# Optimization experiments

Measured on AMD Instinct MI355X. Metric: run time of the kernel, lower is better.

Reference implementation:

```python
import jax, jax.numpy as jnp
import numpy as np

N_NODES = 50000
N_EDGES = 1600000
F_NODE = 8
F_EDGE = 4
HIDDEN = 16
OUT = 8
MLP_HID = 25


def _nnconv(x, src, dst, edge_attr, wa, ba, wb, bb, root, bias, out_ch):
    # edge MLP -> per-edge weight matrix [E, in_ch, out_ch]
    h = jax.nn.relu(edge_attr @ wa + ba) @ wb + bb
    w = h.reshape(-1, x.shape[1], out_ch)
    # gather source node feats, per-edge small matmul
    msg = jnp.einsum('ei,eio->eo', x[src], w)  # [E, out_ch]
    n = x.shape[0]
    agg = jax.ops.segment_sum(msg, dst, num_segments=n)
    cnt = jax.ops.segment_sum(jnp.ones((msg.shape[0],), msg.dtype), dst, num_segments=n)
    agg = agg / jnp.maximum(cnt, 1.0)[:, None]  # mean aggregation
    return agg + x @ root + bias  # root weight + bias (PyG NNConv defaults)


def setup_inputs() -> dict:
    key = jax.random.key(0)
    ks = jax.random.split(key, 16)
    s = lambda k, shape, fan: jax.random.normal(k, shape, jnp.float32) * (1.0 / np.sqrt(fan))
    return {
        'x': jax.random.normal(ks[0], (N_NODES, F_NODE), jnp.float32),
        'edge_index': jax.random.randint(ks[1], (2, N_EDGES), 0, N_NODES),
        'edge_attr': jax.random.normal(ks[2], (N_EDGES, F_EDGE), jnp.float32),
        # conv1 edge-MLP: F_EDGE -> 25 -> F_NODE*HIDDEN
        'w1a': s(ks[3], (F_EDGE, MLP_HID), F_EDGE), 'b1a': jnp.zeros((MLP_HID,), jnp.float32),
        'w1b': s(ks[4], (MLP_HID, F_NODE * HIDDEN), MLP_HID), 'b1b': jnp.zeros((F_NODE * HIDDEN,), jnp.float32),
        'root1': s(ks[5], (F_NODE, HIDDEN), F_NODE), 'bias1': jnp.zeros((HIDDEN,), jnp.float32),
        # conv2 edge-MLP: F_EDGE -> 25 -> HIDDEN*OUT
        'w2a': s(ks[6], (F_EDGE, MLP_HID), F_EDGE), 'b2a': jnp.zeros((MLP_HID,), jnp.float32),
        'w2b': s(ks[7], (MLP_HID, HIDDEN * OUT), MLP_HID), 'b2b': jnp.zeros((HIDDEN * OUT,), jnp.float32),
        'root2': s(ks[8], (HIDDEN, OUT), HIDDEN), 'bias2': jnp.zeros((OUT,), jnp.float32),
    }


def reference(x, edge_index, edge_attr, w1a, b1a, w1b, b1b, root1, bias1,
              w2a, b2a, w2b, b2b, root2, bias2):
    src, dst = edge_index[0], edge_index[1]
    h = _nnconv(x, src, dst, edge_attr, w1a, b1a, w1b, b1b, root1, bias1, HIDDEN)
    h = jax.nn.relu(h)
    # dropout p=0.5 is identity in eval mode
    out = _nnconv(h, src, dst, edge_attr, w2a, b2a, w2b, b2b, root2, bias2, OUT)
    return out
```

## Files before the change

### kernel.cpp

```cpp
#include <hip/hip_runtime.h>
#include <hip/hip_fp16.h>

#define NN 50000
#define NE 1600000
#define FN 8
#define FE 4
#define HID 16
#define OC 8
#define MH 25
#define CAP 80
#define BINS 196
#define BCAP 8960
#define TILE 4096


typedef int iv4 __attribute__((ext_vector_type(4)));
static __device__ __forceinline__ int4 ntload4(const int4* p) {
    iv4 v = __builtin_nontemporal_load(reinterpret_cast<const iv4*>(p));
    return make_int4(v.x, v.y, v.z, v.w);
}
static __device__ __forceinline__ unsigned pack2h(float lo, float hi) {
    return ((unsigned)__half_as_ushort(__float2half_rn(hi)) << 16)
         |  (unsigned)__half_as_ushort(__float2half_rn(lo));
}

#define PKFMA_LO(acc, a, b) \
    asm("v_pk_fma_f16 %0, %1, %2, %0 op_sel:[0,0,0] op_sel_hi:[0,1,1]" \
        : "+v"(acc) : "v"(a), "v"(b))
#define PKFMA_HI(acc, a, b) \
    asm("v_pk_fma_f16 %0, %1, %2, %0 op_sel:[1,0,0] op_sel_hi:[1,1,1]" \
        : "+v"(acc) : "v"(a), "v"(b))
#define PKMAX0(dst, a) \
    asm("v_pk_max_f16 %0, %1, 0" : "=v"(dst) : "v"(a))

static __device__ __forceinline__ void unpack2(unsigned u, float& lo, float& hi) {
    __half2 h; *reinterpret_cast<unsigned*>(&h) = u;
    float2 f = __half22float2(h);
    lo = f.x; hi = f.y;
}

__global__ void __launch_bounds__(256) xhalf_kernel(const float4* __restrict__ x4,
                                                    uint4* __restrict__ xh4) {
    int n = blockIdx.x * 256 + threadIdx.x;
    if (n < NN) {
        float4 a = x4[2 * n], b = x4[2 * n + 1];
        xh4[n] = make_uint4(pack2h(a.x, a.y), pack2h(a.z, a.w),
                            pack2h(b.x, b.y), pack2h(b.z, b.w));
    }
}

__global__ void __launch_bounds__(256) binA_kernel(
    const int* __restrict__ ei, const float* __restrict__ ea,
    unsigned* __restrict__ gcursor, int4* __restrict__ binbuf) {
    __shared__ unsigned hist[BINS], basei[BINS], run[BINS];
    for (int t = threadIdx.x; t < BINS; t += 256) { hist[t] = 0u; run[t] = 0u; }
    __syncthreads();
    const int bb = blockIdx.x * TILE;
    int dsts[16], srcs[16];
    bool actk[4];
#pragma unroll
    for (int k = 0; k < 4; ++k) {
        int e = bb + k * 1024 + threadIdx.x * 4;
        actk[k] = e < NE;
        int4 d = make_int4(0, 0, 0, 0), s = make_int4(0, 0, 0, 0);
        if (actk[k]) {
            d = *reinterpret_cast<const int4*>(ei + NE + e);
            s = *reinterpret_cast<const int4*>(ei + e);
        }
        dsts[4 * k]     = d.x; dsts[4 * k + 1] = d.y;
        dsts[4 * k + 2] = d.z; dsts[4 * k + 3] = d.w;
        srcs[4 * k]     = s.x; srcs[4 * k + 1] = s.y;
        srcs[4 * k + 2] = s.z; srcs[4 * k + 3] = s.w;
        if (actk[k]) {
            atomicAdd(&hist[d.x >> 8], 1u);
            atomicAdd(&hist[d.y >> 8], 1u);
            atomicAdd(&hist[d.z >> 8], 1u);
            atomicAdd(&hist[d.w >> 8], 1u);
        }
    }
    __syncthreads();
    for (int t = threadIdx.x; t < BINS; t += 256)
        basei[t] = hist[t] ? atomicAdd(&gcursor[t], hist[t]) : 0u;
    __syncthreads();
#pragma unroll
    for (int k = 0; k < 4; ++k) {
        if (!actk[k]) continue;
        int e = bb + k * 1024 + threadIdx.x * 4;
#pragma unroll
        for (int j = 0; j < 4; ++j) {
            float4 a = *reinterpret_cast<const float4*>(ea + 4ull * (e + j));
            unsigned u01 = pack2h(a.x, a.y);
            unsigned u23 = pack2h(a.z, a.w);
            int d = dsts[4 * k + j];
            int b = d >> 8;
            unsigned off = atomicAdd(&run[b], 1u);
            unsigned slot = basei[b] + off;
            if (slot < BCAP)
                binbuf[(size_t)b * BCAP + slot] =
                    make_int4(srcs[4 * k + j], d, (int)u01, (int)u23);
        }
    }
}

__global__ void __launch_bounds__(512) binB_kernel(
    const int4* __restrict__ binbuf, const unsigned* __restrict__ gcursor,
    unsigned* __restrict__ cursorF, int4* __restrict__ recs) {
    int b   = blockIdx.x >> 2;
    int sub = blockIdx.x & 3;
    unsigned cnt = gcursor[b];
    if (cnt > BCAP) cnt = BCAP;
    const int4* srcp = binbuf + (size_t)b * BCAP;
    for (unsigned i = threadIdx.x + sub * 512u; i < cnt; i += 2048u) {
        int4 r = ntload4(srcp + i);
        int dst = r.y;
        unsigned pos = atomicAdd(&cursorF[dst], 1u);
        if (pos < CAP)
            recs[(size_t)dst * CAP + pos] = make_int4(r.x, r.z, r.w, 0);
    }
}

__global__ void __launch_bounds__(512, 8) conv1_kernel(
    const float* __restrict__ x, const __half* __restrict__ xh,
    const int4* __restrict__ recs, const unsigned* __restrict__ cnts,
    const float* __restrict__ wa, const float* __restrict__ ba,
    const float* __restrict__ wb, const float* __restrict__ bb,
    const float* __restrict__ root, const float* __restrict__ bias,
    float* __restrict__ hn)
{
    __shared__ float s_wa[FE * MH];
    __shared__ float s_ba[MH];
    __shared__ float s_wb[26 * 129];
    __shared__ float s_root[FN * HID];
    __shared__ float s_bias[HID];
    __shared__ uint2 s_ea[8][4][17];
    __shared__ uint4 s_g[8][4][17];
    for (int t = threadIdx.x; t < FE * MH; t += 512) s_wa[t] = wa[t];
    for (int t = threadIdx.x; t < MH; t += 512) s_ba[t] = ba[t];
    for (int t = threadIdx.x; t < 26 * 128; t += 512) {
        int r = t >> 7, c = t & 127;
        s_wb[r * 129 + c] = (r < MH) ? wb[t] : bb[c];
    }
    for (int t = threadIdx.x; t < FN * HID; t += 512) s_root[t] = root[t];
    for (int t = threadIdx.x; t < HID; t += 512) s_bias[t] = bias[t];
    {
        float* pg = reinterpret_cast<float*>(&s_g[0][0][0]);
        for (int t = threadIdx.x; t < 8 * 4 * 17 * 4; t += 512) pg[t] = 0.f;
    }
    __syncthreads();

    const float4* x4 = reinterpret_cast<const float4*>(x);
    const int w = threadIdx.x >> 6;
    const int l = threadIdx.x & 63;
    const int q = l >> 4;
    const int m = l & 15;
    const int n = blockIdx.x * 32 + w * 4 + q;
    const unsigned cnt = (n < NN) ? cnts[n] : 0u;
    const unsigned lim = cnt < CAP ? cnt : (unsigned)CAP;
    const size_t base = (size_t)n * CAP;
    unsigned cm = lim;
    cm = max(cm, (unsigned)__shfl_xor((int)cm, 16));
    cm = max(cm, (unsigned)__shfl_xor((int)cm, 32));

    const int m2 = m + 16;
    float wB0 = 0.f, wB1 = 0.f, wB2 = 0.f, wB3 = 0.f, bB = 0.f;
    if (m2 < MH) { wB0 = s_wa[m2]; wB1 = s_wa[MH + m2]; wB2 = s_wa[2 * MH + m2];
                   wB3 = s_wa[3 * MH + m2]; bB = s_ba[m2]; }
    else if (m2 == MH) bB = 1.f;
    const unsigned wAB0 = pack2h(s_wa[m], wB0);
    const unsigned wAB1 = pack2h(s_wa[MH + m], wB1);
    const unsigned wAB2 = pack2h(s_wa[2 * MH + m], wB2);
    const unsigned wAB3 = pack2h(s_wa[3 * MH + m], wB3);
    const unsigned bAB  = pack2h(s_ba[m], bB);

    unsigned TA[4] = {0u,0u,0u,0u}, TB[4] = {0u,0u,0u,0u};
    for (unsigned c = 0; c < cm; c += 16) {
        if (c + (unsigned)m < lim) {
            int4 r = ntload4(&recs[base + c + m]);
            s_ea[w][q][m] = make_uint2((unsigned)r.y, (unsigned)r.z);
            s_g[w][q][m] = *reinterpret_cast<const uint4*>(xh + 8ull * r.x);
        }
        asm volatile("s_waitcnt lgkmcnt(0)" ::: "memory");
#pragma unroll 4
        for (int j = 0; j < 16; ++j) {
            uint2 eu = s_ea[w][q][j];
            uint4 gu = s_g[w][q][j];
            unsigned hm2 = bAB;
            PKFMA_LO(hm2, eu.x, wAB0);
            PKFMA_HI(hm2, eu.x, wAB1);
            PKFMA_LO(hm2, eu.y, wAB2);
            PKFMA_HI(hm2, eu.y, wAB3);
            PKMAX0(hm2, hm2);
            bool act = (c + (unsigned)j) < lim;
            hm2 = act ? hm2 : 0u;
            PKFMA_LO(TA[0], hm2, gu.x); PKFMA_LO(TA[1], hm2, gu.y);
            PKFMA_LO(TA[2], hm2, gu.z); PKFMA_LO(TA[3], hm2, gu.w);
            PKFMA_HI(TB[0], hm2, gu.x); PKFMA_HI(TB[1], hm2, gu.y);
            PKFMA_HI(TB[2], hm2, gu.z); PKFMA_HI(TB[3], hm2, gu.w);
        }
        asm volatile("" ::: "memory");
    }

    float T[8], U[8];
    unpack2(TA[0], T[0], T[1]); unpack2(TA[1], T[2], T[3]);
    unpack2(TA[2], T[4], T[5]); unpack2(TA[3], T[6], T[7]);
    unpack2(TB[0], U[0], U[1]); unpack2(TB[1], U[2], U[3]);
    unpack2(TB[2], U[4], U[5]); unpack2(TB[3], U[6], U[7]);

    const int rb = (m2 <= MH) ? m2 : MH;
    float s[16];
#pragma unroll
    for (int o = 0; o < 16; ++o) {
        const float* wv = s_wb + m * 129 + o;
        const float* wu = s_wb + rb * 129 + o;
        float pm = T[0]*wv[0]  + T[1]*wv[16] + T[2]*wv[32] + T[3]*wv[48]
                 + T[4]*wv[64] + T[5]*wv[80] + T[6]*wv[96] + T[7]*wv[112]
                 + U[0]*wu[0]  + U[1]*wu[16] + U[2]*wu[32] + U[3]*wu[48]
                 + U[4]*wu[64] + U[5]*wu[80] + U[6]*wu[96] + U[7]*wu[112];
        pm += __shfl_xor(pm, 8, 16);
        pm += __shfl_xor(pm, 4, 16);
        pm += __shfl_xor(pm, 2, 16);
        pm += __shfl_xor(pm, 1, 16);
        s[o] = pm;
    }

    if (m == 0 && n < NN) {
        float inv = 1.f / fmaxf((float)cnt, 1.f);
        float4 xa = x4[2 * n], xb = x4[2 * n + 1];
        float xn[8] = {xa.x, xa.y, xa.z, xa.w, xb.x, xb.y, xb.z, xb.w};
        float v[16];
#pragma unroll
        for (int o = 0; o < 16; ++o) {
            float r = s[o] * inv + s_bias[o];
#pragma unroll
            for (int i = 0; i < 8; ++i) r += xn[i] * s_root[i * HID + o];
            v[o] = fmaxf(r, 0.f);
        }
        float4* hp = reinterpret_cast<float4*>(hn + 16ull * n);
        hp[0] = make_float4(v[0], v[1], v[2], v[3]);
        hp[1] = make_float4(v[4], v[5], v[6], v[7]);
        hp[2] = make_float4(v[8], v[9], v[10], v[11]);
        hp[3] = make_float4(v[12], v[13], v[14], v[15]);
    }
}

__global__ void __launch_bounds__(256) hn2h_kernel(const float4* __restrict__ hn4,
                                                   uint4* __restrict__ hh4) {
    int n = blockIdx.x * 256 + threadIdx.x;
    if (n < NN) {
        float4 a = hn4[4 * n],     b = hn4[4 * n + 1];
        float4 c = hn4[4 * n + 2], d = hn4[4 * n + 3];
        hh4[2 * n]     = make_uint4(pack2h(a.x, a.y), pack2h(a.z, a.w),
                                    pack2h(b.x, b.y), pack2h(b.z, b.w));
        hh4[2 * n + 1] = make_uint4(pack2h(c.x, c.y), pack2h(c.z, c.w),
                                    pack2h(d.x, d.y), pack2h(d.z, d.w));
    }
}

__global__ void __launch_bounds__(512, 8) conv2_kernel(
    const __half* __restrict__ hh, const int4* __restrict__ recs,
    const unsigned* __restrict__ cnts,
    const float* __restrict__ wa, const float* __restrict__ ba,
    const float* __restrict__ wb, const float* __restrict__ bb,
    const float* __restrict__ root, const float* __restrict__ bias,
    float* __restrict__ out)
{
    __shared__ float s_wa[FE * MH];
    __shared__ float s_ba[MH];
    __shared__ float s_wb[26 * 129];
    __shared__ float s_root[HID * OC];
    __shared__ float s_bias[OC];
    __shared__ uint2 s_ea[8][4][17];
    __shared__ uint4 s_gA[8][4][17];
    __shared__ uint4 s_gB[8][4][17];
    for (int t = threadIdx.x; t < FE * MH; t += 512) s_wa[t] = wa[t];
    for (int t = threadIdx.x; t < MH; t += 512) s_ba[t] = ba[t];
    for (int t = threadIdx.x; t < 26 * 128; t += 512) {
        int r = t >> 7, c = t & 127;
        s_wb[r * 129 + c] = (r < MH) ? wb[t] : bb[c];
    }
    for (int t = threadIdx.x; t < HID * OC; t += 512) s_root[t] = root[t];
    for (int t = threadIdx.x; t < OC; t += 512) s_bias[t] = bias[t];
    {
        float* pg = reinterpret_cast<float*>(&s_gA[0][0][0]);
        for (int t = threadIdx.x; t < 8 * 4 * 17 * 4; t += 512) pg[t] = 0.f;
        float* ph = reinterpret_cast<float*>(&s_gB[0][0][0]);
        for (int t = threadIdx.x; t < 8 * 4 * 17 * 4; t += 512) ph[t] = 0.f;
    }
    __syncthreads();

    const int w = threadIdx.x >> 6;
    const int l = threadIdx.x & 63;
    const int q = l >> 4;
    const int m = l & 15;
    const int n = blockIdx.x * 32 + w * 4 + q;
    const unsigned cnt = (n < NN) ? cnts[n] : 0u;
    const unsigned lim = cnt < CAP ? cnt : (unsigned)CAP;
    const size_t base = (size_t)n * CAP;
    unsigned cm = lim;
    cm = max(cm, (unsigned)__shfl_xor((int)cm, 16));
    cm = max(cm, (unsigned)__shfl_xor((int)cm, 32));

    const int m2 = m + 16;
    float wB0 = 0.f, wB1 = 0.f, wB2 = 0.f, wB3 = 0.f, bB = 0.f;
    if (m2 < MH) { wB0 = s_wa[m2]; wB1 = s_wa[MH + m2]; wB2 = s_wa[2 * MH + m2];
                   wB3 = s_wa[3 * MH + m2]; bB = s_ba[m2]; }
    else if (m2 == MH) bB = 1.f;
    const unsigned wAB0 = pack2h(s_wa[m], wB0);
    const unsigned wAB1 = pack2h(s_wa[MH + m], wB1);
    const unsigned wAB2 = pack2h(s_wa[2 * MH + m], wB2);
    const unsigned wAB3 = pack2h(s_wa[3 * MH + m], wB3);
    const unsigned bAB  = pack2h(s_ba[m], bB);

    unsigned TA[8] = {0u,0u,0u,0u,0u,0u,0u,0u};
    unsigned TB[8] = {0u,0u,0u,0u,0u,0u,0u,0u};
    for (unsigned c = 0; c < cm; c += 16) {
        if (c + (unsigned)m < lim) {
            int4 r = ntload4(&recs[base + c + m]);
            s_ea[w][q][m] = make_uint2((unsigned)r.y, (unsigned)r.z);
            const uint4* gp = reinterpret_cast<const uint4*>(hh + 16ull * r.x);
            s_gA[w][q][m] = gp[0];
            s_gB[w][q][m] = gp[1];
        }
        asm volatile("s_waitcnt lgkmcnt(0)" ::: "memory");
#pragma unroll 4
        for (int j = 0; j < 16; ++j) {
            uint2 eu = s_ea[w][q][j];
            uint4 ga = s_gA[w][q][j];
            uint4 gb = s_gB[w][q][j];
            unsigned hm2 = bAB;
            PKFMA_LO(hm2, eu.x, wAB0);
            PKFMA_HI(hm2, eu.x, wAB1);
            PKFMA_LO(hm2, eu.y, wAB2);
            PKFMA_HI(hm2, eu.y, wAB3);
            PKMAX0(hm2, hm2);
            bool act = (c + (unsigned)j) < lim;
            hm2 = act ? hm2 : 0u;
            PKFMA_LO(TA[0], hm2, ga.x); PKFMA_LO(TA[1], hm2, ga.y);
            PKFMA_LO(TA[2], hm2, ga.z); PKFMA_LO(TA[3], hm2, ga.w);
            PKFMA_LO(TA[4], hm2, gb.x); PKFMA_LO(TA[5], hm2, gb.y);
            PKFMA_LO(TA[6], hm2, gb.z); PKFMA_LO(TA[7], hm2, gb.w);
            PKFMA_HI(TB[0], hm2, ga.x); PKFMA_HI(TB[1], hm2, ga.y);
            PKFMA_HI(TB[2], hm2, ga.z); PKFMA_HI(TB[3], hm2, ga.w);
            PKFMA_HI(TB[4], hm2, gb.x); PKFMA_HI(TB[5], hm2, gb.y);
            PKFMA_HI(TB[6], hm2, gb.z); PKFMA_HI(TB[7], hm2, gb.w);
        }
        asm volatile("" ::: "memory");
    }

    float T[16], U[16];
#pragma unroll
    for (int i = 0; i < 8; ++i) {
        unpack2(TA[i], T[2 * i], T[2 * i + 1]);
        unpack2(TB[i], U[2 * i], U[2 * i + 1]);
    }

    const int rb = (m2 <= MH) ? m2 : MH;
    float s[8];
#pragma unroll
    for (int o = 0; o < 8; ++o) {
        const float* wv = s_wb + m * 129 + o;
        const float* wu = s_wb + rb * 129 + o;
        float pm = 0.f;
#pragma unroll
        for (int i = 0; i < 16; ++i) pm += T[i] * wv[i * 8];
#pragma unroll
        for (int i = 0; i < 16; ++i) pm += U[i] * wu[i * 8];
        pm += __shfl_xor(pm, 8, 16);
        pm += __shfl_xor(pm, 4, 16);
        pm += __shfl_xor(pm, 2, 16);
        pm += __shfl_xor(pm, 1, 16);
        s[o] = pm;
    }

    if (m == 0 && n < NN) {
        float inv = 1.f / fmaxf((float)cnt, 1.f);
        uint4 ha4 = *reinterpret_cast<const uint4*>(hh + 16ull * n);
        uint4 hb4 = *reinterpret_cast<const uint4*>(hh + 16ull * n + 8);
        const __half2* ap = reinterpret_cast<const __half2*>(&ha4);
        const __half2* bp = reinterpret_cast<const __half2*>(&hb4);
        float hnn[16];
#pragma unroll
        for (int i = 0; i < 4; ++i) {
            float2 fa = __half22float2(ap[i]);
            float2 fb = __half22float2(bp[i]);
            hnn[2 * i] = fa.x; hnn[2 * i + 1] = fa.y;
            hnn[8 + 2 * i] = fb.x; hnn[8 + 2 * i + 1] = fb.y;
        }
        float v[8];
#pragma unroll
        for (int o = 0; o < 8; ++o) {
            float r = s[o] * inv + s_bias[o];
#pragma unroll
            for (int i = 0; i < 16; ++i) r += hnn[i] * s_root[i * OC + o];
            v[o] = r;
        }
        float4* op = reinterpret_cast<float4*>(out + 8ull * n);
        op[0] = make_float4(v[0], v[1], v[2], v[3]);
        op[1] = make_float4(v[4], v[5], v[6], v[7]);
    }
}

extern "C" void kernel_launch(void* const* d_in, const int* in_sizes, int n_in,
                              void* d_out, int out_size, void* d_ws, size_t ws_size,
                              hipStream_t stream) {
    const float* x     = (const float*)d_in[0];
    const int*   ei    = (const int*)d_in[1];
    const float* ea    = (const float*)d_in[2];
    const float* w1a   = (const float*)d_in[3];
    const float* b1a   = (const float*)d_in[4];
    const float* w1b   = (const float*)d_in[5];
    const float* b1b   = (const float*)d_in[6];
    const float* root1 = (const float*)d_in[7];
    const float* bias1 = (const float*)d_in[8];
    const float* w2a   = (const float*)d_in[9];
    const float* b2a   = (const float*)d_in[10];
    const float* w2b   = (const float*)d_in[11];
    const float* b2b   = (const float*)d_in[12];
    const float* root2 = (const float*)d_in[13];
    const float* bias2 = (const float*)d_in[14];
    float* out = (float*)d_out;

    char* ws = (char*)d_ws;
    int4*     recs    = (int4*)(ws);
    unsigned* cursorF = (unsigned*)(ws + 64000000);
    unsigned* gcursor = (unsigned*)(ws + 64200000);
    float*    hn      = (float*)(ws + 64200800);
    __half*   hnh     = (__half*)(ws + 67400800);
    __half*   xh      = (__half*)(ws + 69000800);
    int4*     binbuf  = (int4*)(ws + 69800800);

    hipMemsetAsync(ws + 64000000, 0, 200784, stream);
    xhalf_kernel<<<(NN + 255) / 256, 256, 0, stream>>>((const float4*)x, (uint4*)xh);
    binA_kernel<<<(NE + TILE - 1) / TILE, 256, 0, stream>>>(ei, ea, gcursor, binbuf);
    binB_kernel<<<BINS * 4, 512, 0, stream>>>(binbuf, gcursor, cursorF, recs);
    conv1_kernel<<<(NN + 31) / 32, 512, 0, stream>>>(x, xh, recs, cursorF,
                                                     w1a, b1a, w1b, b1b, root1, bias1, hn);
    hn2h_kernel<<<(NN + 255) / 256, 256, 0, stream>>>((const float4*)hn, (uint4*)hnh);
    conv2_kernel<<<(NN + 31) / 32, 512, 0, stream>>>(hnh, recs, cursorF,
                                                     w2a, b2a, w2b, b2b, root2, bias2, out);
}
```

Before: 183.1 us.

## Stage binned edge records in LDS to coalesce binA scatter writes

binA now does a local prefix scan over the per-bin histogram and first scatters each tile's records into a shared-memory staging buffer grouped by bin. It then writes them out in bin order, so consecutive threads store to contiguous slots of each bin's global region instead of scattered addresses. Block size doubles to 512 threads with fewer edges per thread. The 64KB LDS stage and the extra barriers can lower occupancy.

Measured after the change: 177.7 us, median of 2. 1.03x faster.

```diff
diff --git a/kernel.cpp b/kernel.cpp
--- a/kernel.cpp
+++ b/kernel.cpp
@@ -49,18 +49,22 @@
     }
 }
 
-__global__ void __launch_bounds__(256) binA_kernel(
+__global__ void __launch_bounds__(512) binA_kernel(
     const int* __restrict__ ei, const float* __restrict__ ea,
     unsigned* __restrict__ gcursor, int4* __restrict__ binbuf) {
-    __shared__ unsigned hist[BINS], basei[BINS], run[BINS];
-    for (int t = threadIdx.x; t < BINS; t += 256) { hist[t] = 0u; run[t] = 0u; }
-    __syncthreads();
+    __shared__ unsigned hist[256], lstart[256], run[256], basei[256];
+    __shared__ unsigned scanbuf[256];
+    __shared__ int4 stage[TILE];
+    for (int t = threadIdx.x; t < 256; t += 512) { hist[t] = 0u; run[t] = 0u; }
+    __syncthreads();
+
     const int bb = blockIdx.x * TILE;
-    int dsts[16], srcs[16];
-    bool actk[4];
-#pragma unroll
-    for (int k = 0; k < 4; ++k) {
-        int e = bb + k * 1024 + threadIdx.x * 4;
+    const int tid = threadIdx.x;
+    int dsts[8], srcs[8];
+    bool actk[2];
+#pragma unroll
+    for (int k = 0; k < 2; ++k) {
+        int e = bb + k * 2048 + tid * 4;
         actk[k] = e < NE;
         int4 d = make_int4(0, 0, 0, 0), s = make_int4(0, 0, 0, 0);
         if (actk[k]) {
@@ -79,13 +83,23 @@
         }
     }
     __syncthreads();
-    for (int t = threadIdx.x; t < BINS; t += 256)
-        basei[t] = hist[t] ? atomicAdd(&gcursor[t], hist[t]) : 0u;
-    __syncthreads();
-#pragma unroll
-    for (int k = 0; k < 4; ++k) {
+    if (tid < 256) scanbuf[tid] = hist[tid];
+    __syncthreads();
+    for (int off = 1; off < 256; off <<= 1) {
+        unsigned v = 0u;
+        if (tid < 256 && tid >= off) v = scanbuf[tid - off];
+        __syncthreads();
+        if (tid < 256) scanbuf[tid] += v;
+        __syncthreads();
+    }
+    if (tid < 256) lstart[tid] = scanbuf[tid] - hist[tid];
+    if (tid < BINS) basei[tid] = hist[tid] ? atomicAdd(&gcursor[tid], hist[tid]) : 0u;
+    __syncthreads();
+
+#pragma unroll
+    for (int k = 0; k < 2; ++k) {
         if (!actk[k]) continue;
-        int e = bb + k * 1024 + threadIdx.x * 4;
+        int e = bb + k * 2048 + tid * 4;
 #pragma unroll
         for (int j = 0; j < 4; ++j) {
             float4 a = *reinterpret_cast<const float4*>(ea + 4ull * (e + j));
@@ -94,11 +108,17 @@
             int d = dsts[4 * k + j];
             int b = d >> 8;
             unsigned off = atomicAdd(&run[b], 1u);
-            unsigned slot = basei[b] + off;
-            if (slot < BCAP)
-                binbuf[(size_t)b * BCAP + slot] =
-                    make_int4(srcs[4 * k + j], d, (int)u01, (int)u23);
-        }
+            stage[lstart[b] + off] = make_int4(srcs[4 * k + j], d, (int)u01, (int)u23);
+        }
+    }
+    __syncthreads();
+
+    const int tot = (bb + TILE <= NE) ? TILE : (NE - bb);
+    for (int i = tid; i < tot; i += 512) {
+        int4 r = stage[i];
+        int b = r.y >> 8;
+        unsigned slot = basei[b] + ((unsigned)i - lstart[b]);
+        if (slot < BCAP) binbuf[(size_t)b * BCAP + slot] = r;
     }
 }
 
@@ -431,7 +451,7 @@
 
     hipMemsetAsync(ws + 64000000, 0, 200784, stream);
     xhalf_kernel<<<(NN + 255) / 256, 256, 0, stream>>>((const float4*)x, (uint4*)xh);
-    binA_kernel<<<(NE + TILE - 1) / TILE, 256, 0, stream>>>(ei, ea, gcursor, binbuf);
+    binA_kernel<<<(NE + TILE - 1) / TILE, 512, 0, stream>>>(ei, ea, gcursor, binbuf);
     binB_kernel<<<BINS * 4, 512, 0, stream>>>(binbuf, gcursor, cursorF, recs);
     conv1_kernel<<<(NN + 31) / 32, 512, 0, stream>>>(x, xh, recs, cursorF,
                                                      w1a, b1a, w1b, b1b, root1, bias1, hn);
```
